# Kernel tuning notes

Measured on AMD Instinct MI355X. Metric: run time of the kernel, lower is better.

Reference implementation:

```python
import jax, jax.numpy as jnp
import numpy as np

N_NODES = 50000
N_EDGES = 800000
NUM_GRAPHS = 512
NEG_SLOPE = 0.2  # PyG GATv2Conv default negative_slope


def setup_inputs() -> dict:
    key = jax.random.key(0)
    ks = jax.random.split(key, 16)
    F_in, H = 128, 2
    C1, C2, NC = 32, 16, 6
    x = jax.random.normal(ks[0], (N_NODES, F_in), dtype=jnp.float32)
    edge_index = jax.random.randint(ks[1], (2, N_EDGES), 0, N_NODES, dtype=jnp.int64)
    batch = jnp.sort(jax.random.randint(ks[2], (N_NODES,), 0, NUM_GRAPHS, dtype=jnp.int64))
    s = lambda fan_in: 1.0 / np.sqrt(fan_in)
    return {
        "x": x, "edge_index": edge_index, "batch": batch,
        # conv1: in=128 -> heads=2, out=32 (concat 64)
        "Wl1": jax.random.normal(ks[3], (F_in, H * C1), jnp.float32) * s(F_in),
        "bl1": jnp.zeros((H * C1,), jnp.float32),
        "Wr1": jax.random.normal(ks[4], (F_in, H * C1), jnp.float32) * s(F_in),
        "att1": jax.random.normal(ks[5], (H, C1), jnp.float32) * s(C1),
        "b1": jnp.zeros((H * C1,), jnp.float32),
        # conv2: in=64 -> heads=2, out=16 (concat 32)
        "Wl2": jax.random.normal(ks[6], (H * C1, H * C2), jnp.float32) * s(H * C1),
        "bl2": jnp.zeros((H * C2,), jnp.float32),
        "Wr2": jax.random.normal(ks[7], (H * C1, H * C2), jnp.float32) * s(H * C1),
        "att2": jax.random.normal(ks[8], (H, C2), jnp.float32) * s(C2),
        "b2": jnp.zeros((H * C2,), jnp.float32),
        # fc: 32 -> 6
        "Wfc": jax.random.normal(ks[9], (H * C2, NC), jnp.float32) * s(H * C2),
        "bfc": jnp.zeros((NC,), jnp.float32),
    }


def _gatv2_conv(x, src, dst, Wl, bl, Wr, att, bias):
    """PyG GATv2Conv (concat heads, add_self_loops already applied to src/dst)."""
    H, C = att.shape
    N = x.shape[0]
    xl = (x @ Wl + bl).reshape(N, H, C)  # source/message transform
    xr = (x @ Wr).reshape(N, H, C)       # target transform
    e = jax.nn.leaky_relu(xl[src] + xr[dst], NEG_SLOPE)  # [E,H,C]
    score = jnp.einsum('ehc,hc->eh', e, att)             # [E,H]
    # segment softmax over edges sharing the same destination node
    smax = jax.ops.segment_max(score, dst, num_segments=N)      # [N,H]
    ex = jnp.exp(score - smax[dst])
    denom = jax.ops.segment_sum(ex, dst, num_segments=N)        # [N,H]
    alpha = ex / denom[dst]                                     # [E,H]
    out = jax.ops.segment_sum(alpha[:, :, None] * xl[src], dst, num_segments=N)
    return out.reshape(N, H * C) + bias


def reference(x, edge_index, batch, Wl1, bl1, Wr1, att1, b1,
              Wl2, bl2, Wr2, att2, b2, Wfc, bfc):
    N = x.shape[0]
    loops = jnp.arange(N, dtype=edge_index.dtype)
    src = jnp.concatenate([edge_index[0], loops])  # add_self_loops=True
    dst = jnp.concatenate([edge_index[1], loops])
    h = jax.nn.elu(_gatv2_conv(x, src, dst, Wl1, bl1, Wr1, att1, b1))
    h = jax.nn.elu(_gatv2_conv(h, src, dst, Wl2, bl2, Wr2, att2, b2))
    # global mean pool over graphs
    sums = jax.ops.segment_sum(h, batch, num_segments=NUM_GRAPHS)
    cnt = jax.ops.segment_sum(jnp.ones((N,), h.dtype), batch, num_segments=NUM_GRAPHS)
    pooled = sums / jnp.maximum(cnt, 1.0)[:, None]
    return jax.nn.log_softmax(pooled @ Wfc + bfc, axis=1)
```

## Files before the change

### kernel.cpp

```cpp
#include <hip/hip_runtime.h>
#include <math.h>

#define N_NODES 50000
#define N_EDGES 800000
#define NUM_GRAPHS 512
#define NEG_SLOPE 0.2f
#define LOG_MD 6
#define ROWCAP 63
#define NBKT 196
#define NPART 200
#define EPB_PART 4000

typedef unsigned short ushort_t;
typedef unsigned int   uint_t;
typedef __attribute__((ext_vector_type(4))) float f32x4;
typedef __attribute__((ext_vector_type(8))) short s16x8;

__device__ __forceinline__ ushort_t f2bf(float f) {
    union { float f; uint_t u; } v; v.f = f;
    uint_t u = v.u;
    return (ushort_t)((u + 0x7fffu + ((u >> 16) & 1u)) >> 16);
}

__device__ __forceinline__ void unpack8(const ushort_t* p, float* f) {
    uint4 u = *(const uint4*)p;
    f[0] = __uint_as_float(u.x << 16); f[1] = __uint_as_float(u.x & 0xffff0000u);
    f[2] = __uint_as_float(u.y << 16); f[3] = __uint_as_float(u.y & 0xffff0000u);
    f[4] = __uint_as_float(u.z << 16); f[5] = __uint_as_float(u.z & 0xffff0000u);
    f[6] = __uint_as_float(u.w << 16); f[7] = __uint_as_float(u.w & 0xffff0000u);
}

__global__ void hist_k(const int* __restrict__ ei_dst, int* __restrict__ bucket_cnt,
                       float* __restrict__ gz) {
    __shared__ int h[NBKT];
    const int tid = threadIdx.x;
    for (int i = tid; i < NBKT; i += 256) h[i] = 0;
    int gt = blockIdx.x * 256 + tid;
    if (gt < NUM_GRAPHS * 33) gz[gt] = 0.f;
    __syncthreads();
    const int base = blockIdx.x * EPB_PART;
    for (int i = tid; i < EPB_PART; i += 256)
        atomicAdd(&h[ei_dst[base + i] >> 8], 1);
    __syncthreads();
    for (int i = tid; i < NBKT; i += 256)
        if (h[i]) atomicAdd(&bucket_cnt[i], h[i]);
}

__global__ void bscan_k(const int* __restrict__ bucket_cnt,
                        int* __restrict__ bucket_off, int* __restrict__ bucket_cur) {
    __shared__ int s[256];
    int tid = threadIdx.x;
    s[tid] = (tid < NBKT) ? bucket_cnt[tid] : 0;
    __syncthreads();
    for (int off = 1; off < 256; off <<= 1) {
        int v = (tid >= off) ? s[tid - off] : 0;
        __syncthreads();
        s[tid] += v;
        __syncthreads();
    }
    if (tid < NBKT) {
        int excl = (tid == 0) ? 0 : s[tid - 1];
        bucket_off[tid] = excl;
        bucket_cur[tid] = excl;
    }
}

__global__ void __launch_bounds__(256) part_k(const int* __restrict__ ei,
                                              int* __restrict__ bucket_cur,
                                              int2* __restrict__ binned) {
    __shared__ int2 ebuf[EPB_PART];
    __shared__ int2 sbuf[EPB_PART];
    __shared__ int hist[NBKT], loff[NBKT], rk[NBKT], gbase[NBKT];
    __shared__ int s2[256];
    const int tid = threadIdx.x;
    for (int i = tid; i < NBKT; i += 256) { hist[i] = 0; rk[i] = 0; }
    __syncthreads();
    const int base = blockIdx.x * EPB_PART;
    for (int i = tid; i < EPB_PART; i += 256) {
        int s = ei[base + i];
        int d = ei[N_EDGES + base + i];
        ebuf[i] = make_int2(s, d);
        atomicAdd(&hist[d >> 8], 1);
    }
    __syncthreads();
    s2[tid] = (tid < NBKT) ? hist[tid] : 0;
    __syncthreads();
    for (int off = 1; off < 256; off <<= 1) {
        int v = (tid >= off) ? s2[tid - off] : 0;
        __syncthreads();
        s2[tid] += v;
        __syncthreads();
    }
    if (tid < NBKT) {
        loff[tid] = (tid == 0) ? 0 : s2[tid - 1];
        gbase[tid] = hist[tid] ? atomicAdd(&bucket_cur[tid], hist[tid]) : 0;
    }
    __syncthreads();
    for (int i = tid; i < EPB_PART; i += 256) {
        int2 e = ebuf[i];
        int b = e.y >> 8;
        int r = atomicAdd(&rk[b], 1);
        sbuf[loff[b] + r] = e;
    }
    __syncthreads();
    for (int i = tid; i < EPB_PART; i += 256) {
        int2 e = sbuf[i];
        int b = e.y >> 8;
        binned[gbase[b] + (i - loff[b])] = e;
    }
}

__global__ void __launch_bounds__(256) build_k(const int* __restrict__ bucket_off,
                                               const int2* __restrict__ binned,
                                               int* __restrict__ col) {
    __shared__ int win[256 * ROWCAP];
    __shared__ int cnt[256];
    const int tid = threadIdx.x;
    for (int i = tid; i < 256 * ROWCAP; i += 256) win[i] = 0;
    if (tid < 256) cnt[tid] = 0;
    __syncthreads();
    const int b = blockIdx.x;
    const int beg = bucket_off[b];
    const int end = (b == NBKT - 1) ? N_EDGES : bucket_off[b + 1];
    for (int i = beg + tid; i < end; i += 256) {
        int2 e = binned[i];
        int row = e.y & 255;
        int c = atomicAdd(&cnt[row], 1);
        if (c < ROWCAP) win[row * ROWCAP + c] = e.x;
    }
    __syncthreads();
    const int n0 = b << 8;
    const int nrows = min(256, N_NODES - n0);
    int* dst = col + ((size_t)n0 << LOG_MD);
    for (int i = tid; i < nrows * 64; i += 256) {
        int row = i >> 6, s = i & 63;
        dst[i] = (s == 63) ? min(cnt[row], ROWCAP) : win[row * ROWCAP + s];
    }
}

__global__ void prep_bt_k(const float* __restrict__ Wl1, const float* __restrict__ Wr1,
                          const float* __restrict__ Wl2, const float* __restrict__ Wr2,
                          ushort_t* __restrict__ Bt1, ushort_t* __restrict__ Bt2) {
    int gid = blockIdx.x * 256 + threadIdx.x;
    if (gid < 16384) {
        int j = gid >> 7, k = gid & 127;
        float v = (j < 64) ? Wl1[k * 64 + j] : Wr1[k * 64 + (j - 64)];
        Bt1[gid] = f2bf(v);
    } else if (gid < 16384 + 4096) {
        int g = gid - 16384;
        int j = g >> 6, k = g & 63;
        float v = (j < 32) ? Wl2[k * 32 + j] : Wr2[k * 32 + (j - 32)];
        Bt2[g] = f2bf(v);
    }
}

__global__ void __launch_bounds__(256) linear1_mfma_k(
        const float* __restrict__ x, const ushort_t* __restrict__ Bt,
        const float* __restrict__ bl,
        ushort_t* __restrict__ xl, ushort_t* __restrict__ xr) {
    __shared__ ushort_t bts[128 * 136];
    const int tid = threadIdx.x;
    {
        const uint_t* src = (const uint_t*)Bt;
        uint_t* dst = (uint_t*)bts;
        for (int i = tid; i < 8192; i += 256) {
            int row = i >> 6, pos = i & 63;
            dst[row * 68 + pos] = src[i];
        }
    }
    __syncthreads();
    const int lane = tid & 63;
    const int wv = tid >> 6;
    const int q = lane >> 4, m = lane & 15;
    const int n0w = blockIdx.x * 64 + wv * 16;
    const int rowA = min(n0w + m, N_NODES - 1);
    const float* xrow = x + (size_t)rowA * 128;

    f32x4 acc[8];
    #pragma unroll
    for (int t = 0; t < 8; ++t) acc[t] = (f32x4){0.f, 0.f, 0.f, 0.f};

    #pragma unroll
    for (int ks = 0; ks < 4; ++ks) {
        const int k0 = ks * 32 + q * 8;
        float4 a0 = *(const float4*)(xrow + k0);
        float4 a1 = *(const float4*)(xrow + k0 + 4);
        s16x8 af;
        af[0] = (short)f2bf(a0.x); af[1] = (short)f2bf(a0.y);
        af[2] = (short)f2bf(a0.z); af[3] = (short)f2bf(a0.w);
        af[4] = (short)f2bf(a1.x); af[5] = (short)f2bf(a1.y);
        af[6] = (short)f2bf(a1.z); af[7] = (short)f2bf(a1.w);
        #pragma unroll
        for (int t = 0; t < 8; ++t) {
            const s16x8 bf = *(const s16x8*)(bts + (t * 16 + m) * 136 + k0);
            acc[t] = __builtin_amdgcn_mfma_f32_16x16x32_bf16(af, bf, acc[t], 0, 0, 0);
        }
    }
    #pragma unroll
    for (int t = 0; t < 8; ++t) {
        int j = t * 16 + m;
        float bias = (t < 4) ? bl[j] : 0.f;
        #pragma unroll
        for (int r = 0; r < 4; ++r) {
            int n = n0w + q * 4 + r;
            if (n < N_NODES) {
                if (t < 4) xl[(size_t)n * 64 + j] = f2bf(acc[t][r] + bias);
                else       xr[(size_t)n * 64 + (j - 64)] = f2bf(acc[t][r]);
            }
        }
    }
}

__global__ void __launch_bounds__(256) linear2_mfma_k(
        const ushort_t* __restrict__ h1, const ushort_t* __restrict__ Bt2,
        const float* __restrict__ bl2,
        ushort_t* __restrict__ xl2, ushort_t* __restrict__ xr2) {
    __shared__ ushort_t bts[64 * 72];
    const int tid = threadIdx.x;
    {
        const uint_t* src = (const uint_t*)Bt2;
        uint_t* dst = (uint_t*)bts;
        for (int i = tid; i < 2048; i += 256) {
            int row = i >> 5, pos = i & 31;
            dst[row * 36 + pos] = src[i];
        }
    }
    __syncthreads();
    const int lane = tid & 63;
    const int wv = tid >> 6;
    const int q = lane >> 4, m = lane & 15;
    const int n0w = blockIdx.x * 64 + wv * 16;
    const int rowA = min(n0w + m, N_NODES - 1);
    const ushort_t* hrow = h1 + (size_t)rowA * 64;

    f32x4 acc[4];
    #pragma unroll
    for (int t = 0; t < 4; ++t) acc[t] = (f32x4){0.f, 0.f, 0.f, 0.f};

    #pragma unroll
    for (int ks = 0; ks < 2; ++ks) {
        const int k0 = ks * 32 + q * 8;
        const s16x8 af = *(const s16x8*)(hrow + k0);
        #pragma unroll
        for (int t = 0; t < 4; ++t) {
            const s16x8 bf = *(const s16x8*)(bts + (t * 16 + m) * 72 + k0);
            acc[t] = __builtin_amdgcn_mfma_f32_16x16x32_bf16(af, bf, acc[t], 0, 0, 0);
        }
    }
    #pragma unroll
    for (int t = 0; t < 4; ++t) {
        int j = t * 16 + m;
        float bias = (t < 2) ? bl2[j] : 0.f;
        #pragma unroll
        for (int r = 0; r < 4; ++r) {
            int n = n0w + q * 4 + r;
            if (n < N_NODES) {
                if (t < 2) xl2[(size_t)n * 32 + j] = f2bf(acc[t][r] + bias);
                else       xr2[(size_t)n * 32 + (j - 32)] = f2bf(acc[t][r]);
            }
        }
    }
}

template<int C2, int LPN, int HEADL, bool OUT_BF16>
__global__ void __launch_bounds__(256) gat_conv_k(
        const int* __restrict__ col,
        const ushort_t* __restrict__ xl, const ushort_t* __restrict__ xr,
        const float* __restrict__ att, const float* __restrict__ b,
        void* __restrict__ outp) {
    const int NPW = 64 / LPN;
    int wave = (blockIdx.x * blockDim.x + threadIdx.x) >> 6;
    int lane = threadIdx.x & 63;
    int slot = lane / LPN;
    int c8   = lane % LPN;
    int n = wave * NPW + slot;
    const bool nvalid = (n < N_NODES);
    const int nn = nvalid ? n : (N_NODES - 1);

    float xrv[8], attv[8], bv[8];
    unpack8(xr + (size_t)nn * C2 + c8 * 8, xrv);
    *(float4*)(attv)     = ((const float4*)att)[c8 * 2];
    *(float4*)(attv + 4) = ((const float4*)att)[c8 * 2 + 1];
    *(float4*)(bv)       = ((const float4*)b)[c8 * 2];
    *(float4*)(bv + 4)   = ((const float4*)b)[c8 * 2 + 1];

    const int start = nn << LOG_MD;
    const int dg = nvalid ? min(col[start + 63], ROWCAP) : 0;

    float den, acc[8];
    {
        float xsv[8];
        unpack8(xl + (size_t)nn * C2 + c8 * 8, xsv);
        float p = 0.f;
        #pragma unroll
        for (int i = 0; i < 8; ++i) {
            float z = xsv[i] + xrv[i];
            z = (z >= 0.f) ? z : NEG_SLOPE * z;
            p = fmaf(z, attv[i], p);
        }
        #pragma unroll
        for (int off = HEADL / 2; off > 0; off >>= 1)
            p += __shfl_xor(p, off, 64);
        float ex = __expf(fminf(p, 80.f));
        den = ex;
        #pragma unroll
        for (int i = 0; i < 8; ++i) acc[i] = ex * xsv[i];
    }

    int mdg = dg;
    #pragma unroll
    for (int off = 32; off > 0; off >>= 1) mdg = max(mdg, __shfl_xor(mdg, off, 64));

    uint4 raw = *(const uint4*)(xl + (size_t)col[start] * C2 + c8 * 8);
    for (int k = 0; k < mdg; ++k) {
        uint4 cu = raw;
        if (k + 1 < mdg) {
            int kk = min(k + 1, dg - 1);
            if (kk < 0) kk = 0;
            int sn = col[start + kk];
            raw = *(const uint4*)(xl + (size_t)sn * C2 + c8 * 8);
        }
        float xv[8];
        xv[0] = __uint_as_float(cu.x << 16); xv[1] = __uint_as_float(cu.x & 0xffff0000u);
        xv[2] = __uint_as_float(cu.y << 16); xv[3] = __uint_as_float(cu.y & 0xffff0000u);
        xv[4] = __uint_as_float(cu.z << 16); xv[5] = __uint_as_float(cu.z & 0xffff0000u);
        xv[6] = __uint_as_float(cu.w << 16); xv[7] = __uint_as_float(cu.w & 0xffff0000u);
        float p = 0.f;
        #pragma unroll
        for (int i = 0; i < 8; ++i) {
            float z = xv[i] + xrv[i];
            z = (z >= 0.f) ? z : NEG_SLOPE * z;
            p = fmaf(z, attv[i], p);
        }
        #pragma unroll
        for (int off = HEADL / 2; off > 0; off >>= 1)
            p += __shfl_xor(p, off, 64);
        float ex = (k < dg) ? __expf(fminf(p, 80.f)) : 0.f;
        den += ex;
        #pragma unroll
        for (int i = 0; i < 8; ++i) acc[i] = fmaf(ex, xv[i], acc[i]);
    }
    if (nvalid) {
        float inv = 1.f / den;
        float o[8];
        #pragma unroll
        for (int i = 0; i < 8; ++i) {
            float v = fmaf(acc[i], inv, bv[i]);
            o[i] = (v > 0.f) ? v : (__expf(v) - 1.f);
        }
        if (OUT_BF16) {
            uint4 u;
            u.x = ((uint_t)f2bf(o[1]) << 16) | f2bf(o[0]);
            u.y = ((uint_t)f2bf(o[3]) << 16) | f2bf(o[2]);
            u.z = ((uint_t)f2bf(o[5]) << 16) | f2bf(o[4]);
            u.w = ((uint_t)f2bf(o[7]) << 16) | f2bf(o[6]);
            ((uint4*)outp)[(size_t)n * (C2 / 8) + c8] = u;
        } else {
            float4* op = (float4*)outp;
            op[(size_t)n * (C2 / 4) + c8 * 2]     = *(float4*)o;
            op[(size_t)n * (C2 / 4) + c8 * 2 + 1] = *(float4*)(o + 4);
        }
    }
}

__global__ void pool_k(const float* __restrict__ h2, const int* __restrict__ batch,
                       float* __restrict__ gsum, float* __restrict__ gcnt) {
    const int NCH = (N_NODES + 7) / 8;
    int t = blockIdx.x * blockDim.x + threadIdx.x;
    if (t >= NCH * 32) return;
    int c = t & 31;
    int n0 = (t >> 5) * 8;
    int nend = min(n0 + 8, N_NODES);
    int curb = batch[n0];
    float s = 0.f, cnt = 0.f;
    for (int n = n0; n < nend; ++n) {
        int bb = batch[n];
        if (bb != curb) {
            atomicAdd(gsum + (size_t)curb * 32 + c, s);
            if (c == 0) atomicAdd(gcnt + curb, cnt);
            s = 0.f; cnt = 0.f; curb = bb;
        }
        s += h2[(size_t)n * 32 + c];
        cnt += 1.f;
    }
    atomicAdd(gsum + (size_t)curb * 32 + c, s);
    if (c == 0) atomicAdd(gcnt + curb, cnt);
}

__global__ void head_k(const float* __restrict__ gsum, const float* __restrict__ gcnt,
                       const float* __restrict__ Wfc, const float* __restrict__ bfc,
                       float* __restrict__ out) {
    int gph = blockIdx.x * blockDim.x + threadIdx.x;
    if (gph >= NUM_GRAPHS) return;
    float inv = 1.f / fmaxf(gcnt[gph], 1.f);
    float logits[6];
    #pragma unroll
    for (int j = 0; j < 6; ++j) logits[j] = bfc[j];
    for (int k = 0; k < 32; ++k) {
        float p = gsum[(size_t)gph * 32 + k] * inv;
        #pragma unroll
        for (int j = 0; j < 6; ++j) logits[j] = fmaf(p, Wfc[k * 6 + j], logits[j]);
    }
    float m = logits[0];
    #pragma unroll
    for (int j = 1; j < 6; ++j) m = fmaxf(m, logits[j]);
    float ssum = 0.f;
    #pragma unroll
    for (int j = 0; j < 6; ++j) ssum += expf(logits[j] - m);
    float lse = m + logf(ssum);
    #pragma unroll
    for (int j = 0; j < 6; ++j) out[(size_t)gph * 6 + j] = logits[j] - lse;
}

extern "C" void kernel_launch(void* const* d_in, const int* in_sizes, int n_in,
                              void* d_out, int out_size, void* d_ws, size_t ws_size,
                              hipStream_t stream) {
    const float* x    = (const float*)d_in[0];
    const int*   ei   = (const int*)d_in[1];
    const int*   batch= (const int*)d_in[2];
    const float* Wl1  = (const float*)d_in[3];
    const float* bl1  = (const float*)d_in[4];
    const float* Wr1  = (const float*)d_in[5];
    const float* att1 = (const float*)d_in[6];
    const float* b1   = (const float*)d_in[7];
    const float* Wl2  = (const float*)d_in[8];
    const float* bl2  = (const float*)d_in[9];
    const float* Wr2  = (const float*)d_in[10];
    const float* att2 = (const float*)d_in[11];
    const float* b2   = (const float*)d_in[12];
    const float* Wfc  = (const float*)d_in[13];
    const float* bfc  = (const float*)d_in[14];
    float* out = (float*)d_out;

    char* wsp = (char*)d_ws;
    ushort_t* xl1 = (ushort_t*)wsp; wsp += (size_t)N_NODES * 64 * 2;
    ushort_t* xr1 = (ushort_t*)wsp; wsp += (size_t)N_NODES * 64 * 2;
    ushort_t* h1  = (ushort_t*)wsp; wsp += (size_t)N_NODES * 64 * 2;
    ushort_t* xl2 = (ushort_t*)wsp; wsp += (size_t)N_NODES * 32 * 2;
    ushort_t* xr2 = (ushort_t*)wsp; wsp += (size_t)N_NODES * 32 * 2;
    float* h2   = (float*)wsp; wsp += (size_t)N_NODES * 32 * 4;
    float* gsum = (float*)wsp; wsp += (size_t)NUM_GRAPHS * 32 * 4;
    float* gcnt = (float*)wsp; wsp += (size_t)NUM_GRAPHS * 4;
    int* col    = (int*)wsp; wsp += ((size_t)N_NODES << LOG_MD) * 4;
    int* bucket_cnt = (int*)wsp; wsp += NBKT * 4;
    int* bucket_off = (int*)wsp; wsp += NBKT * 4;
    int* bucket_cur = (int*)wsp; wsp += NBKT * 4;
    wsp += 16 - ((size_t)wsp & 15);
    ushort_t* Bt1 = (ushort_t*)wsp; wsp += 128 * 128 * 2;
    ushort_t* Bt2 = (ushort_t*)wsp; wsp += 64 * 64 * 2;
    int2* binned = (int2*)h1;

    const int TB = 256;

    hipMemsetAsync(bucket_cnt, 0, NBKT * sizeof(int), stream);
    prep_bt_k<<<80, 256, 0, stream>>>(Wl1, Wr1, Wl2, Wr2, Bt1, Bt2);
    hist_k<<<NPART, 256, 0, stream>>>(ei + N_EDGES, bucket_cnt, gsum);
    bscan_k<<<1, 256, 0, stream>>>(bucket_cnt, bucket_off, bucket_cur);
    part_k<<<NPART, 256, 0, stream>>>(ei, bucket_cur, binned);
    build_k<<<NBKT, 256, 0, stream>>>(bucket_off, binned, col);

    linear1_mfma_k<<<(N_NODES + 63) / 64, 256, 0, stream>>>(x, Bt1, bl1, xl1, xr1);
    {
        int waves = (N_NODES + 7) / 8;
        gat_conv_k<64, 8, 4, true><<<(waves + 3) / 4, 256, 0, stream>>>(
            col, xl1, xr1, att1, b1, h1);
    }

    linear2_mfma_k<<<(N_NODES + 63) / 64, 256, 0, stream>>>(h1, Bt2, bl2, xl2, xr2);
    {
        int waves = (N_NODES + 15) / 16;
        gat_conv_k<32, 4, 2, false><<<(waves + 3) / 4, 256, 0, stream>>>(
            col, xl2, xr2, att2, b2, h2);
    }

    pool_k<<<(((N_NODES + 7) / 8) * 32 + TB - 1) / TB, TB, 0, stream>>>(h2, batch, gsum, gcnt);
    head_k<<<(NUM_GRAPHS + TB - 1) / TB, TB, 0, stream>>>(gsum, gcnt, Wfc, bfc, out);
}
```

Baseline: 217.4 us.

## Merge CSR build into a cooperative kernel and fuse conv2 with mean pooling

The memset, weight-prep, histogram, scan, partition and CSR-build kernels become one cooperative kernel with grid-wide syncs. A shared-memory union lets the partition and build phases reuse the same space. The second GAT convolution now writes its ELU outputs straight into per-graph sums with atomics, which removes the fp32 h2 buffer and the separate pool kernel. Node counts per graph are gathered in the cooperative kernel. The aim is fewer launches and less round-trip memory traffic, at the cost of grid-sync overhead and heavy atomic contention on the 512x32 pooled sums.

```diff
diff --git a/kernel.cpp b/kernel.cpp
--- a/kernel.cpp
+++ b/kernel.cpp
@@ -1,5 +1,8 @@
 #include <hip/hip_runtime.h>
+#include <hip/hip_cooperative_groups.h>
 #include <math.h>
+
+namespace cg = cooperative_groups;
 
 #define N_NODES 50000
 #define N_EDGES 800000
@@ -30,127 +33,123 @@
     f[6] = __uint_as_float(u.w << 16); f[7] = __uint_as_float(u.w & 0xffff0000u);
 }
 
-__global__ void hist_k(const int* __restrict__ ei_dst, int* __restrict__ bucket_cnt,
-                       float* __restrict__ gz) {
-    __shared__ int h[NBKT];
+__global__ void __launch_bounds__(256) csr_coop_k(
+        const int* __restrict__ ei, const int* __restrict__ batch,
+        const float* __restrict__ Wl1, const float* __restrict__ Wr1,
+        const float* __restrict__ Wl2, const float* __restrict__ Wr2,
+        ushort_t* __restrict__ Bt1, ushort_t* __restrict__ Bt2,
+        int* __restrict__ bucket_cnt, int* __restrict__ bucket_off,
+        int* __restrict__ bucket_cur,
+        int2* __restrict__ binned, int* __restrict__ col,
+        float* __restrict__ gz ) {
+    cg::grid_group grid = cg::this_grid();
+    __shared__ int hloc[NBKT];
+    union U {
+        struct { int2 ebuf[EPB_PART]; int2 sbuf[EPB_PART];
+                 int loff[NBKT]; int rk[NBKT]; int gbase[NBKT]; int s2[256]; } p;
+        struct { int win[256 * ROWCAP]; int cnt[256]; } b;
+    };
+    __shared__ U u;
     const int tid = threadIdx.x;
-    for (int i = tid; i < NBKT; i += 256) h[i] = 0;
-    int gt = blockIdx.x * 256 + tid;
+    const int blk = blockIdx.x;
+    const int gt = blk * 256 + tid;
+
+    if (gt < NBKT) bucket_cnt[gt] = 0;
     if (gt < NUM_GRAPHS * 33) gz[gt] = 0.f;
+    if (gt < 16384) {
+        int j = gt >> 7, k = gt & 127;
+        float v = (j < 64) ? Wl1[k * 64 + j] : Wr1[k * 64 + (j - 64)];
+        Bt1[gt] = f2bf(v);
+    } else if (gt < 16384 + 4096) {
+        int g = gt - 16384;
+        int j = g >> 6, k = g & 63;
+        float v = (j < 32) ? Wl2[k * 32 + j] : Wr2[k * 32 + (j - 32)];
+        Bt2[g] = f2bf(v);
+    }
+    for (int i = tid; i < NBKT; i += 256) hloc[i] = 0;
     __syncthreads();
-    const int base = blockIdx.x * EPB_PART;
-    for (int i = tid; i < EPB_PART; i += 256)
-        atomicAdd(&h[ei_dst[base + i] >> 8], 1);
-    __syncthreads();
-    for (int i = tid; i < NBKT; i += 256)
-        if (h[i]) atomicAdd(&bucket_cnt[i], h[i]);
-}
-
-__global__ void bscan_k(const int* __restrict__ bucket_cnt,
-                        int* __restrict__ bucket_off, int* __restrict__ bucket_cur) {
-    __shared__ int s[256];
-    int tid = threadIdx.x;
-    s[tid] = (tid < NBKT) ? bucket_cnt[tid] : 0;
-    __syncthreads();
-    for (int off = 1; off < 256; off <<= 1) {
-        int v = (tid >= off) ? s[tid - off] : 0;
-        __syncthreads();
-        s[tid] += v;
-        __syncthreads();
-    }
-    if (tid < NBKT) {
-        int excl = (tid == 0) ? 0 : s[tid - 1];
-        bucket_off[tid] = excl;
-        bucket_cur[tid] = excl;
-    }
-}
-
-__global__ void __launch_bounds__(256) part_k(const int* __restrict__ ei,
-                                              int* __restrict__ bucket_cur,
-                                              int2* __restrict__ binned) {
-    __shared__ int2 ebuf[EPB_PART];
-    __shared__ int2 sbuf[EPB_PART];
-    __shared__ int hist[NBKT], loff[NBKT], rk[NBKT], gbase[NBKT];
-    __shared__ int s2[256];
-    const int tid = threadIdx.x;
-    for (int i = tid; i < NBKT; i += 256) { hist[i] = 0; rk[i] = 0; }
-    __syncthreads();
-    const int base = blockIdx.x * EPB_PART;
+    const int base = blk * EPB_PART;
     for (int i = tid; i < EPB_PART; i += 256) {
         int s = ei[base + i];
         int d = ei[N_EDGES + base + i];
-        ebuf[i] = make_int2(s, d);
-        atomicAdd(&hist[d >> 8], 1);
-    }
-    __syncthreads();
-    s2[tid] = (tid < NBKT) ? hist[tid] : 0;
+        u.p.ebuf[i] = make_int2(s, d);
+        atomicAdd(&hloc[d >> 8], 1);
+    }
+    grid.sync();
+
+    for (int i = tid; i < NBKT; i += 256)
+        if (hloc[i]) atomicAdd(&bucket_cnt[i], hloc[i]);
+    {
+        int node = blk * 250 + tid;
+        if (tid < 250) atomicAdd(&gz[NUM_GRAPHS * 32 + batch[node]], 1.f);
+    }
+    grid.sync();
+
+    if (blk == 0) {
+        u.p.s2[tid] = (tid < NBKT) ? bucket_cnt[tid] : 0;
+        __syncthreads();
+        for (int off = 1; off < 256; off <<= 1) {
+            int v = (tid >= off) ? u.p.s2[tid - off] : 0;
+            __syncthreads();
+            u.p.s2[tid] += v;
+            __syncthreads();
+        }
+        if (tid < NBKT) {
+            int excl = (tid == 0) ? 0 : u.p.s2[tid - 1];
+            bucket_off[tid] = excl;
+            bucket_cur[tid] = excl;
+        }
+    }
+    grid.sync();
+
+    for (int i = tid; i < NBKT; i += 256) u.p.rk[i] = 0;
+    u.p.s2[tid] = (tid < NBKT) ? hloc[tid] : 0;
     __syncthreads();
     for (int off = 1; off < 256; off <<= 1) {
-        int v = (tid >= off) ? s2[tid - off] : 0;
+        int v = (tid >= off) ? u.p.s2[tid - off] : 0;
         __syncthreads();
-        s2[tid] += v;
+        u.p.s2[tid] += v;
         __syncthreads();
     }
     if (tid < NBKT) {
-        loff[tid] = (tid == 0) ? 0 : s2[tid - 1];
-        gbase[tid] = hist[tid] ? atomicAdd(&bucket_cur[tid], hist[tid]) : 0;
+        u.p.loff[tid] = (tid == 0) ? 0 : u.p.s2[tid - 1];
+        u.p.gbase[tid] = hloc[tid] ? atomicAdd(&bucket_cur[tid], hloc[tid]) : 0;
     }
     __syncthreads();
     for (int i = tid; i < EPB_PART; i += 256) {
-        int2 e = ebuf[i];
-        int b = e.y >> 8;
-        int r = atomicAdd(&rk[b], 1);
-        sbuf[loff[b] + r] = e;
+        int2 e = u.p.ebuf[i];
+        int bb = e.y >> 8;
+        int r = atomicAdd(&u.p.rk[bb], 1);
+        u.p.sbuf[u.p.loff[bb] + r] = e;
     }
     __syncthreads();
     for (int i = tid; i < EPB_PART; i += 256) {
-        int2 e = sbuf[i];
-        int b = e.y >> 8;
-        binned[gbase[b] + (i - loff[b])] = e;
-    }
-}
-
-__global__ void __launch_bounds__(256) build_k(const int* __restrict__ bucket_off,
-                                               const int2* __restrict__ binned,
-                                               int* __restrict__ col) {
-    __shared__ int win[256 * ROWCAP];
-    __shared__ int cnt[256];
-    const int tid = threadIdx.x;
-    for (int i = tid; i < 256 * ROWCAP; i += 256) win[i] = 0;
-    if (tid < 256) cnt[tid] = 0;
-    __syncthreads();
-    const int b = blockIdx.x;
-    const int beg = bucket_off[b];
-    const int end = (b == NBKT - 1) ? N_EDGES : bucket_off[b + 1];
-    for (int i = beg + tid; i < end; i += 256) {
-        int2 e = binned[i];
-        int row = e.y & 255;
-        int c = atomicAdd(&cnt[row], 1);
-        if (c < ROWCAP) win[row * ROWCAP + c] = e.x;
-    }
-    __syncthreads();
-    const int n0 = b << 8;
-    const int nrows = min(256, N_NODES - n0);
-    int* dst = col + ((size_t)n0 << LOG_MD);
-    for (int i = tid; i < nrows * 64; i += 256) {
-        int row = i >> 6, s = i & 63;
-        dst[i] = (s == 63) ? min(cnt[row], ROWCAP) : win[row * ROWCAP + s];
-    }
-}
-
-__global__ void prep_bt_k(const float* __restrict__ Wl1, const float* __restrict__ Wr1,
-                          const float* __restrict__ Wl2, const float* __restrict__ Wr2,
-                          ushort_t* __restrict__ Bt1, ushort_t* __restrict__ Bt2) {
-    int gid = blockIdx.x * 256 + threadIdx.x;
-    if (gid < 16384) {
-        int j = gid >> 7, k = gid & 127;
-        float v = (j < 64) ? Wl1[k * 64 + j] : Wr1[k * 64 + (j - 64)];
-        Bt1[gid] = f2bf(v);
-    } else if (gid < 16384 + 4096) {
-        int g = gid - 16384;
-        int j = g >> 6, k = g & 63;
-        float v = (j < 32) ? Wl2[k * 32 + j] : Wr2[k * 32 + (j - 32)];
-        Bt2[g] = f2bf(v);
+        int2 e = u.p.sbuf[i];
+        int bb = e.y >> 8;
+        binned[u.p.gbase[bb] + (i - u.p.loff[bb])] = e;
+    }
+    grid.sync();
+
+    if (blk < NBKT) {
+        for (int i = tid; i < 256 * ROWCAP; i += 256) u.b.win[i] = 0;
+        u.b.cnt[tid] = 0;
+        __syncthreads();
+        const int beg = bucket_off[blk];
+        const int end = (blk == NBKT - 1) ? N_EDGES : bucket_off[blk + 1];
+        for (int i = beg + tid; i < end; i += 256) {
+            int2 e = binned[i];
+            int row = e.y & 255;
+            int c = atomicAdd(&u.b.cnt[row], 1);
+            if (c < ROWCAP) u.b.win[row * ROWCAP + c] = e.x;
+        }
+        __syncthreads();
+        const int n0 = blk << 8;
+        const int nrows = min(256, N_NODES - n0);
+        int* dst = col + ((size_t)n0 << LOG_MD);
+        for (int i = tid; i < nrows * 64; i += 256) {
+            int row = i >> 6, s = i & 63;
+            dst[i] = (s == 63) ? min(u.b.cnt[row], ROWCAP) : u.b.win[row * ROWCAP + s];
+        }
     }
 }
 
@@ -262,12 +261,12 @@
     }
 }
 
-template<int C2, int LPN, int HEADL, bool OUT_BF16>
+template<int C2, int LPN, int HEADL>
 __global__ void __launch_bounds__(256) gat_conv_k(
         const int* __restrict__ col,
         const ushort_t* __restrict__ xl, const ushort_t* __restrict__ xr,
         const float* __restrict__ att, const float* __restrict__ b,
-        void* __restrict__ outp) {
+        ushort_t* __restrict__ outp) {
     const int NPW = 64 / LPN;
     int wave = (blockIdx.x * blockDim.x + threadIdx.x) >> 6;
     int lane = threadIdx.x & 63;
@@ -348,43 +347,100 @@
             float v = fmaf(acc[i], inv, bv[i]);
             o[i] = (v > 0.f) ? v : (__expf(v) - 1.f);
         }
-        if (OUT_BF16) {
-            uint4 u;
-            u.x = ((uint_t)f2bf(o[1]) << 16) | f2bf(o[0]);
-            u.y = ((uint_t)f2bf(o[3]) << 16) | f2bf(o[2]);
-            u.z = ((uint_t)f2bf(o[5]) << 16) | f2bf(o[4]);
-            u.w = ((uint_t)f2bf(o[7]) << 16) | f2bf(o[6]);
-            ((uint4*)outp)[(size_t)n * (C2 / 8) + c8] = u;
-        } else {
-            float4* op = (float4*)outp;
-            op[(size_t)n * (C2 / 4) + c8 * 2]     = *(float4*)o;
-            op[(size_t)n * (C2 / 4) + c8 * 2 + 1] = *(float4*)(o + 4);
-        }
-    }
-}
-
-__global__ void pool_k(const float* __restrict__ h2, const int* __restrict__ batch,
-                       float* __restrict__ gsum, float* __restrict__ gcnt) {
-    const int NCH = (N_NODES + 7) / 8;
-    int t = blockIdx.x * blockDim.x + threadIdx.x;
-    if (t >= NCH * 32) return;
-    int c = t & 31;
-    int n0 = (t >> 5) * 8;
-    int nend = min(n0 + 8, N_NODES);
-    int curb = batch[n0];
-    float s = 0.f, cnt = 0.f;
-    for (int n = n0; n < nend; ++n) {
-        int bb = batch[n];
-        if (bb != curb) {
-            atomicAdd(gsum + (size_t)curb * 32 + c, s);
-            if (c == 0) atomicAdd(gcnt + curb, cnt);
-            s = 0.f; cnt = 0.f; curb = bb;
-        }
-        s += h2[(size_t)n * 32 + c];
-        cnt += 1.f;
-    }
-    atomicAdd(gsum + (size_t)curb * 32 + c, s);
-    if (c == 0) atomicAdd(gcnt + curb, cnt);
+        uint4 u;
+        u.x = ((uint_t)f2bf(o[1]) << 16) | f2bf(o[0]);
+        u.y = ((uint_t)f2bf(o[3]) << 16) | f2bf(o[2]);
+        u.z = ((uint_t)f2bf(o[5]) << 16) | f2bf(o[4]);
+        u.w = ((uint_t)f2bf(o[7]) << 16) | f2bf(o[6]);
+        ((uint4*)outp)[(size_t)n * (C2 / 8) + c8] = u;
+    }
+}
+
+__global__ void __launch_bounds__(256) gat_conv2_pool_k(
+        const int* __restrict__ col,
+        const ushort_t* __restrict__ xl, const ushort_t* __restrict__ xr,
+        const float* __restrict__ att, const float* __restrict__ b,
+        const int* __restrict__ batch, float* __restrict__ gsum) {
+    const int C2 = 32, LPN = 4, HEADL = 2;
+    const int NPW = 64 / LPN;
+    int wave = (blockIdx.x * blockDim.x + threadIdx.x) >> 6;
+    int lane = threadIdx.x & 63;
+    int slot = lane / LPN;
+    int c8   = lane % LPN;
+    int n = wave * NPW + slot;
+    const bool nvalid = (n < N_NODES);
+    const int nn = nvalid ? n : (N_NODES - 1);
+
+    float xrv[8], attv[8], bv[8];
+    unpack8(xr + (size_t)nn * C2 + c8 * 8, xrv);
+    *(float4*)(attv)     = ((const float4*)att)[c8 * 2];
+    *(float4*)(attv + 4) = ((const float4*)att)[c8 * 2 + 1];
+    *(float4*)(bv)       = ((const float4*)b)[c8 * 2];
+    *(float4*)(bv + 4)   = ((const float4*)b)[c8 * 2 + 1];
+
+    const int start = nn << LOG_MD;
+    const int dg = nvalid ? min(col[start + 63], ROWCAP) : 0;
+
+    float den, acc[8];
+    {
+        float xsv[8];
+        unpack8(xl + (size_t)nn * C2 + c8 * 8, xsv);
+        float p = 0.f;
+        #pragma unroll
+        for (int i = 0; i < 8; ++i) {
+            float z = xsv[i] + xrv[i];
+            z = (z >= 0.f) ? z : NEG_SLOPE * z;
+            p = fmaf(z, attv[i], p);
+        }
+        p += __shfl_xor(p, 1, 64);
+        float ex = __expf(fminf(p, 80.f));
+        den = ex;
+        #pragma unroll
+        for (int i = 0; i < 8; ++i) acc[i] = ex * xsv[i];
+    }
+
+    int mdg = dg;
+    #pragma unroll
+    for (int off = 32; off > 0; off >>= 1) mdg = max(mdg, __shfl_xor(mdg, off, 64));
+
+    uint4 raw = *(const uint4*)(xl + (size_t)col[start] * C2 + c8 * 8);
+    for (int k = 0; k < mdg; ++k) {
+        uint4 cu = raw;
+        if (k + 1 < mdg) {
+            int kk = min(k + 1, dg - 1);
+            if (kk < 0) kk = 0;
+            int sn = col[start + kk];
+            raw = *(const uint4*)(xl + (size_t)sn * C2 + c8 * 8);
+        }
+        float xv[8];
+        xv[0] = __uint_as_float(cu.x << 16); xv[1] = __uint_as_float(cu.x & 0xffff0000u);
+        xv[2] = __uint_as_float(cu.y << 16); xv[3] = __uint_as_float(cu.y & 0xffff0000u);
+        xv[4] = __uint_as_float(cu.z << 16); xv[5] = __uint_as_float(cu.z & 0xffff0000u);
+        xv[6] = __uint_as_float(cu.w << 16); xv[7] = __uint_as_float(cu.w & 0xffff0000u);
+        float p = 0.f;
+        #pragma unroll
+        for (int i = 0; i < 8; ++i) {
+            float z = xv[i] + xrv[i];
+            z = (z >= 0.f) ? z : NEG_SLOPE * z;
+            p = fmaf(z, attv[i], p);
+        }
+        p += __shfl_xor(p, 1, 64);
+        float ex = (k < dg) ? __expf(fminf(p, 80.f)) : 0.f;
+        den += ex;
+        #pragma unroll
+        for (int i = 0; i < 8; ++i) acc[i] = fmaf(ex, xv[i], acc[i]);
+    }
+    if (nvalid) {
+        float inv = 1.f / den;
+        int bg = batch[n];
+        float* gp = gsum + (size_t)bg * 32 + c8 * 8;
+        #pragma unroll
+        for (int i = 0; i < 8; ++i) {
+            float v = fmaf(acc[i], inv, bv[i]);
+            v = (v > 0.f) ? v : (__expf(v) - 1.f);
+            atomicAdd(gp + i, v);
+        }
+    }
 }
 
 __global__ void head_k(const float* __restrict__ gsum, const float* __restrict__ gcnt,
@@ -438,7 +494,6 @@
     ushort_t* h1  = (ushort_t*)wsp; wsp += (size_t)N_NODES * 64 * 2;
     ushort_t* xl2 = (ushort_t*)wsp; wsp += (size_t)N_NODES * 32 * 2;
     ushort_t* xr2 = (ushort_t*)wsp; wsp += (size_t)N_NODES * 32 * 2;
-    float* h2   = (float*)wsp; wsp += (size_t)N_NODES * 32 * 4;
     float* gsum = (float*)wsp; wsp += (size_t)NUM_GRAPHS * 32 * 4;
     float* gcnt = (float*)wsp; wsp += (size_t)NUM_GRAPHS * 4;
     int* col    = (int*)wsp; wsp += ((size_t)N_NODES << LOG_MD) * 4;
@@ -450,29 +505,31 @@
     ushort_t* Bt2 = (ushort_t*)wsp; wsp += 64 * 64 * 2;
     int2* binned = (int2*)h1;
 
-    const int TB = 256;
-
-    hipMemsetAsync(bucket_cnt, 0, NBKT * sizeof(int), stream);
-    prep_bt_k<<<80, 256, 0, stream>>>(Wl1, Wr1, Wl2, Wr2, Bt1, Bt2);
-    hist_k<<<NPART, 256, 0, stream>>>(ei + N_EDGES, bucket_cnt, gsum);
-    bscan_k<<<1, 256, 0, stream>>>(bucket_cnt, bucket_off, bucket_cur);
-    part_k<<<NPART, 256, 0, stream>>>(ei, bucket_cur, binned);
-    build_k<<<NBKT, 256, 0, stream>>>(bucket_off, binned, col);
+    {
+        void* args[] = {
+            (void*)&ei, (void*)&batch,
+            (void*)&Wl1, (void*)&Wr1, (void*)&Wl2, (void*)&Wr2,
+            (void*)&Bt1, (void*)&Bt2,
+            (void*)&bucket_cnt, (void*)&bucket_off, (void*)&bucket_cur,
+            (void*)&binned, (void*)&col, (void*)&gsum,
+        };
+        hipLaunchCooperativeKernel((const void*)csr_coop_k,
+                                   dim3(NPART), dim3(256), args, 0, stream);
+    }
 
     linear1_mfma_k<<<(N_NODES + 63) / 64, 256, 0, stream>>>(x, Bt1, bl1, xl1, xr1);
     {
         int waves = (N_NODES + 7) / 8;
-        gat_conv_k<64, 8, 4, true><<<(waves + 3) / 4, 256, 0, stream>>>(
+        gat_conv_k<64, 8, 4><<<(waves + 3) / 4, 256, 0, stream>>>(
             col, xl1, xr1, att1, b1, h1);
     }
 
     linear2_mfma_k<<<(N_NODES + 63) / 64, 256, 0, stream>>>(h1, Bt2, bl2, xl2, xr2);
     {
         int waves = (N_NODES + 15) / 16;
-        gat_conv_k<32, 4, 2, false><<<(waves + 3) / 4, 256, 0, stream>>>(
-            col, xl2, xr2, att2, b2, h2);
-    }
-
-    pool_k<<<(((N_NODES + 7) / 8) * 32 + TB - 1) / TB, TB, 0, stream>>>(h2, batch, gsum, gcnt);
-    head_k<<<(NUM_GRAPHS + TB - 1) / TB, TB, 0, stream>>>(gsum, gcnt, Wfc, bfc, out);
-}
+        gat_conv2_pool_k<<<(waves + 3) / 4, 256, 0, stream>>>(
+            col, xl2, xr2, att2, b2, batch, gsum);
+    }
+
+    head_k<<<(NUM_GRAPHS + 255) / 256, 256, 0, stream>>>(gsum, gcnt, Wfc, bfc, out);
+}
```

After: 412.7 us. 89.8% more time.

## Drop histogram/scan pre-pass via fixed-capacity buckets and fold node counting into partition

Applied to the files above, without the earlier changes.

Removes the hist and scan kernels and the memset. Each destination bucket now gets a fixed BCAP-sized region, filled through atomic cursors, and edges past the capacity are dropped. The weight bf16 transpose and the zeroing are fused into one kernel, and per-graph node counts move from pool_k into part_k. The GAT aggregation loop now runs each lane to its own degree instead of the wave-max degree, which cuts masked iterations but adds divergence. The fixed capacity assumes buckets never exceed 5120 edges, which holds only for roughly uniform destinations.

```diff
diff --git a/kernel.cpp b/kernel.cpp
--- a/kernel.cpp
+++ b/kernel.cpp
@@ -10,6 +10,7 @@
 #define NBKT 196
 #define NPART 200
 #define EPB_PART 4000
+#define BCAP 5120
 
 typedef unsigned short ushort_t;
 typedef unsigned int   uint_t;
@@ -30,44 +31,30 @@
     f[6] = __uint_as_float(u.w << 16); f[7] = __uint_as_float(u.w & 0xffff0000u);
 }
 
-__global__ void hist_k(const int* __restrict__ ei_dst, int* __restrict__ bucket_cnt,
-                       float* __restrict__ gz) {
-    __shared__ int h[NBKT];
-    const int tid = threadIdx.x;
-    for (int i = tid; i < NBKT; i += 256) h[i] = 0;
-    int gt = blockIdx.x * 256 + tid;
+__global__ void zero_prep_k(const float* __restrict__ Wl1, const float* __restrict__ Wr1,
+                            const float* __restrict__ Wl2, const float* __restrict__ Wr2,
+                            ushort_t* __restrict__ Bt1, ushort_t* __restrict__ Bt2,
+                            int* __restrict__ bucket_cur, float* __restrict__ gz) {
+    int gt = blockIdx.x * 256 + threadIdx.x;
+    if (gt < NBKT) bucket_cur[gt] = 0;
     if (gt < NUM_GRAPHS * 33) gz[gt] = 0.f;
-    __syncthreads();
-    const int base = blockIdx.x * EPB_PART;
-    for (int i = tid; i < EPB_PART; i += 256)
-        atomicAdd(&h[ei_dst[base + i] >> 8], 1);
-    __syncthreads();
-    for (int i = tid; i < NBKT; i += 256)
-        if (h[i]) atomicAdd(&bucket_cnt[i], h[i]);
-}
-
-__global__ void bscan_k(const int* __restrict__ bucket_cnt,
-                        int* __restrict__ bucket_off, int* __restrict__ bucket_cur) {
-    __shared__ int s[256];
-    int tid = threadIdx.x;
-    s[tid] = (tid < NBKT) ? bucket_cnt[tid] : 0;
-    __syncthreads();
-    for (int off = 1; off < 256; off <<= 1) {
-        int v = (tid >= off) ? s[tid - off] : 0;
-        __syncthreads();
-        s[tid] += v;
-        __syncthreads();
-    }
-    if (tid < NBKT) {
-        int excl = (tid == 0) ? 0 : s[tid - 1];
-        bucket_off[tid] = excl;
-        bucket_cur[tid] = excl;
+    if (gt < 16384) {
+        int j = gt >> 7, k = gt & 127;
+        float v = (j < 64) ? Wl1[k * 64 + j] : Wr1[k * 64 + (j - 64)];
+        Bt1[gt] = f2bf(v);
+    } else if (gt < 16384 + 4096) {
+        int g = gt - 16384;
+        int j = g >> 6, k = g & 63;
+        float v = (j < 32) ? Wl2[k * 32 + j] : Wr2[k * 32 + (j - 32)];
+        Bt2[g] = f2bf(v);
     }
 }
 
 __global__ void __launch_bounds__(256) part_k(const int* __restrict__ ei,
+                                              const int* __restrict__ batch,
                                               int* __restrict__ bucket_cur,
-                                              int2* __restrict__ binned) {
+                                              int2* __restrict__ binned,
+                                              float* __restrict__ gz) {
     __shared__ int2 ebuf[EPB_PART];
     __shared__ int2 sbuf[EPB_PART];
     __shared__ int hist[NBKT], loff[NBKT], rk[NBKT], gbase[NBKT];
@@ -82,6 +69,10 @@
         ebuf[i] = make_int2(s, d);
         atomicAdd(&hist[d >> 8], 1);
     }
+    {
+        int node = blockIdx.x * 250 + tid;
+        if (tid < 250) atomicAdd(&gz[NUM_GRAPHS * 32 + batch[node]], 1.f);
+    }
     __syncthreads();
     s2[tid] = (tid < NBKT) ? hist[tid] : 0;
     __syncthreads();
@@ -106,24 +97,25 @@
     for (int i = tid; i < EPB_PART; i += 256) {
         int2 e = sbuf[i];
         int b = e.y >> 8;
-        binned[gbase[b] + (i - loff[b])] = e;
-    }
-}
-
-__global__ void __launch_bounds__(256) build_k(const int* __restrict__ bucket_off,
+        int slot = gbase[b] + (i - loff[b]);
+        if (slot < BCAP) binned[(size_t)b * BCAP + slot] = e;
+    }
+}
+
+__global__ void __launch_bounds__(256) build_k(const int* __restrict__ bucket_cur,
                                                const int2* __restrict__ binned,
                                                int* __restrict__ col) {
     __shared__ int win[256 * ROWCAP];
     __shared__ int cnt[256];
     const int tid = threadIdx.x;
     for (int i = tid; i < 256 * ROWCAP; i += 256) win[i] = 0;
-    if (tid < 256) cnt[tid] = 0;
+    cnt[tid] = 0;
     __syncthreads();
     const int b = blockIdx.x;
-    const int beg = bucket_off[b];
-    const int end = (b == NBKT - 1) ? N_EDGES : bucket_off[b + 1];
-    for (int i = beg + tid; i < end; i += 256) {
-        int2 e = binned[i];
+    const int total = min(bucket_cur[b], BCAP);
+    const int2* src = binned + (size_t)b * BCAP;
+    for (int i = tid; i < total; i += 256) {
+        int2 e = src[i];
         int row = e.y & 255;
         int c = atomicAdd(&cnt[row], 1);
         if (c < ROWCAP) win[row * ROWCAP + c] = e.x;
@@ -135,22 +127,6 @@
     for (int i = tid; i < nrows * 64; i += 256) {
         int row = i >> 6, s = i & 63;
         dst[i] = (s == 63) ? min(cnt[row], ROWCAP) : win[row * ROWCAP + s];
-    }
-}
-
-__global__ void prep_bt_k(const float* __restrict__ Wl1, const float* __restrict__ Wr1,
-                          const float* __restrict__ Wl2, const float* __restrict__ Wr2,
-                          ushort_t* __restrict__ Bt1, ushort_t* __restrict__ Bt2) {
-    int gid = blockIdx.x * 256 + threadIdx.x;
-    if (gid < 16384) {
-        int j = gid >> 7, k = gid & 127;
-        float v = (j < 64) ? Wl1[k * 64 + j] : Wr1[k * 64 + (j - 64)];
-        Bt1[gid] = f2bf(v);
-    } else if (gid < 16384 + 4096) {
-        int g = gid - 16384;
-        int j = g >> 6, k = g & 63;
-        float v = (j < 32) ? Wl2[k * 32 + j] : Wr2[k * 32 + (j - 32)];
-        Bt2[g] = f2bf(v);
     }
 }
 
@@ -307,38 +283,34 @@
         for (int i = 0; i < 8; ++i) acc[i] = ex * xsv[i];
     }
 
-    int mdg = dg;
-    #pragma unroll
-    for (int off = 32; off > 0; off >>= 1) mdg = max(mdg, __shfl_xor(mdg, off, 64));
-
-    uint4 raw = *(const uint4*)(xl + (size_t)col[start] * C2 + c8 * 8);
-    for (int k = 0; k < mdg; ++k) {
-        uint4 cu = raw;
-        if (k + 1 < mdg) {
-            int kk = min(k + 1, dg - 1);
-            if (kk < 0) kk = 0;
-            int sn = col[start + kk];
-            raw = *(const uint4*)(xl + (size_t)sn * C2 + c8 * 8);
-        }
-        float xv[8];
-        xv[0] = __uint_as_float(cu.x << 16); xv[1] = __uint_as_float(cu.x & 0xffff0000u);
-        xv[2] = __uint_as_float(cu.y << 16); xv[3] = __uint_as_float(cu.y & 0xffff0000u);
-        xv[4] = __uint_as_float(cu.z << 16); xv[5] = __uint_as_float(cu.z & 0xffff0000u);
-        xv[6] = __uint_as_float(cu.w << 16); xv[7] = __uint_as_float(cu.w & 0xffff0000u);
-        float p = 0.f;
-        #pragma unroll
-        for (int i = 0; i < 8; ++i) {
-            float z = xv[i] + xrv[i];
-            z = (z >= 0.f) ? z : NEG_SLOPE * z;
-            p = fmaf(z, attv[i], p);
-        }
-        #pragma unroll
-        for (int off = HEADL / 2; off > 0; off >>= 1)
-            p += __shfl_xor(p, off, 64);
-        float ex = (k < dg) ? __expf(fminf(p, 80.f)) : 0.f;
-        den += ex;
-        #pragma unroll
-        for (int i = 0; i < 8; ++i) acc[i] = fmaf(ex, xv[i], acc[i]);
+    if (dg > 0) {
+        uint4 raw = *(const uint4*)(xl + (size_t)col[start] * C2 + c8 * 8);
+        for (int k = 0; k < dg; ++k) {
+            uint4 cu = raw;
+            if (k + 1 < dg) {
+                int sn = col[start + k + 1];
+                raw = *(const uint4*)(xl + (size_t)sn * C2 + c8 * 8);
+            }
+            float xv[8];
+            xv[0] = __uint_as_float(cu.x << 16); xv[1] = __uint_as_float(cu.x & 0xffff0000u);
+            xv[2] = __uint_as_float(cu.y << 16); xv[3] = __uint_as_float(cu.y & 0xffff0000u);
+            xv[4] = __uint_as_float(cu.z << 16); xv[5] = __uint_as_float(cu.z & 0xffff0000u);
+            xv[6] = __uint_as_float(cu.w << 16); xv[7] = __uint_as_float(cu.w & 0xffff0000u);
+            float p = 0.f;
+            #pragma unroll
+            for (int i = 0; i < 8; ++i) {
+                float z = xv[i] + xrv[i];
+                z = (z >= 0.f) ? z : NEG_SLOPE * z;
+                p = fmaf(z, attv[i], p);
+            }
+            #pragma unroll
+            for (int off = HEADL / 2; off > 0; off >>= 1)
+                p += __shfl_xor(p, off, 64);
+            float ex = __expf(fminf(p, 80.f));
+            den += ex;
+            #pragma unroll
+            for (int i = 0; i < 8; ++i) acc[i] = fmaf(ex, xv[i], acc[i]);
+        }
     }
     if (nvalid) {
         float inv = 1.f / den;
@@ -364,7 +336,7 @@
 }
 
 __global__ void pool_k(const float* __restrict__ h2, const int* __restrict__ batch,
-                       float* __restrict__ gsum, float* __restrict__ gcnt) {
+                       float* __restrict__ gsum, float* __restrict__ gcnt_unused) {
     const int NCH = (N_NODES + 7) / 8;
     int t = blockIdx.x * blockDim.x + threadIdx.x;
     if (t >= NCH * 32) return;
@@ -372,19 +344,16 @@
     int n0 = (t >> 5) * 8;
     int nend = min(n0 + 8, N_NODES);
     int curb = batch[n0];
-    float s = 0.f, cnt = 0.f;
+    float s = 0.f;
     for (int n = n0; n < nend; ++n) {
         int bb = batch[n];
         if (bb != curb) {
             atomicAdd(gsum + (size_t)curb * 32 + c, s);
-            if (c == 0) atomicAdd(gcnt + curb, cnt);
-            s = 0.f; cnt = 0.f; curb = bb;
+            s = 0.f; curb = bb;
         }
         s += h2[(size_t)n * 32 + c];
-        cnt += 1.f;
     }
     atomicAdd(gsum + (size_t)curb * 32 + c, s);
-    if (c == 0) atomicAdd(gcnt + curb, cnt);
 }
 
 __global__ void head_k(const float* __restrict__ gsum, const float* __restrict__ gcnt,
@@ -442,22 +411,15 @@
     float* gsum = (float*)wsp; wsp += (size_t)NUM_GRAPHS * 32 * 4;
     float* gcnt = (float*)wsp; wsp += (size_t)NUM_GRAPHS * 4;
     int* col    = (int*)wsp; wsp += ((size_t)N_NODES << LOG_MD) * 4;
-    int* bucket_cnt = (int*)wsp; wsp += NBKT * 4;
-    int* bucket_off = (int*)wsp; wsp += NBKT * 4;
     int* bucket_cur = (int*)wsp; wsp += NBKT * 4;
     wsp += 16 - ((size_t)wsp & 15);
     ushort_t* Bt1 = (ushort_t*)wsp; wsp += 128 * 128 * 2;
     ushort_t* Bt2 = (ushort_t*)wsp; wsp += 64 * 64 * 2;
-    int2* binned = (int2*)h1;
-
-    const int TB = 256;
-
-    hipMemsetAsync(bucket_cnt, 0, NBKT * sizeof(int), stream);
-    prep_bt_k<<<80, 256, 0, stream>>>(Wl1, Wr1, Wl2, Wr2, Bt1, Bt2);
-    hist_k<<<NPART, 256, 0, stream>>>(ei + N_EDGES, bucket_cnt, gsum);
-    bscan_k<<<1, 256, 0, stream>>>(bucket_cnt, bucket_off, bucket_cur);
-    part_k<<<NPART, 256, 0, stream>>>(ei, bucket_cur, binned);
-    build_k<<<NBKT, 256, 0, stream>>>(bucket_off, binned, col);
+    int2* binned = (int2*)xl1;
+
+    zero_prep_k<<<80, 256, 0, stream>>>(Wl1, Wr1, Wl2, Wr2, Bt1, Bt2, bucket_cur, gsum);
+    part_k<<<NPART, 256, 0, stream>>>(ei, batch, bucket_cur, binned, gsum);
+    build_k<<<NBKT, 256, 0, stream>>>(bucket_cur, binned, col);
 
     linear1_mfma_k<<<(N_NODES + 63) / 64, 256, 0, stream>>>(x, Bt1, bl1, xl1, xr1);
     {
@@ -473,6 +435,6 @@
             col, xl2, xr2, att2, b2, h2);
     }
 
-    pool_k<<<(((N_NODES + 7) / 8) * 32 + TB - 1) / TB, TB, 0, stream>>>(h2, batch, gsum, gcnt);
-    head_k<<<(NUM_GRAPHS + TB - 1) / TB, TB, 0, stream>>>(gsum, gcnt, Wfc, bfc, out);
-}
+    pool_k<<<(((N_NODES + 7) / 8) * 32 + 255) / 256, 256, 0, stream>>>(h2, batch, gsum, gcnt);
+    head_k<<<(NUM_GRAPHS + 255) / 256, 256, 0, stream>>>(gsum, gcnt, Wfc, bfc, out);
+}
```

Result: slower. 230.3 us (+5.9%).
